# Performance work log

Measured on AMD Instinct MI355X. Metric: run time of the kernel, lower is better.

The kernel has to match this reference:

```python
import jax, jax.numpy as jnp
import numpy as np

B, L, H, NH = 8, 1024, 1024, 16
HD = H // NH  # head_dim = 64
SCALE = HD ** -0.5


def setup_inputs() -> dict:
    key = jax.random.key(0)
    kx, kqkv, kw, kb = jax.random.split(key, 4)
    x = jax.random.normal(kx, (B, L, H), dtype=jnp.float32)
    # nn.Linear(H, 3H, bias=False): weight [3H, H]
    w_qkv = jax.random.normal(kqkv, (3 * H, H), dtype=jnp.float32) * (H ** -0.5)
    # out_proj: nn.Linear(H, H) with bias
    w_out = jax.random.normal(kw, (H, H), dtype=jnp.float32) * (H ** -0.5)
    b_out = jax.random.normal(kb, (H,), dtype=jnp.float32) * 0.01
    return {"x": x, "w_qkv": w_qkv, "w_out": w_out, "b_out": b_out}


def reference(x, w_qkv, w_out, b_out):
    # qkv projection: [B, L, 3H]
    qkv = jnp.einsum('bld,ed->ble', x, w_qkv)
    # rearrange 'b l (qkv h d) -> qkv b h l d'
    qkv = qkv.reshape(B, L, 3, NH, HD)
    q = qkv[:, :, 0].transpose(0, 2, 1, 3)  # [B, NH, L, HD]
    k = qkv[:, :, 1].transpose(0, 2, 1, 3)
    v = qkv[:, :, 2].transpose(0, 2, 1, 3)
    att = jnp.einsum('bhxd,bhyd->bhxy', q, k) * SCALE
    att = jax.nn.softmax(att, axis=-1)
    o = jnp.einsum('bhxy,bhyd->bhxd', att, v)  # [B, NH, L, HD]
    o = o.transpose(0, 2, 1, 3).reshape(B, L, H)
    return jnp.einsum('bld,ed->ble', o, w_out) + b_out
```

## Files before the change

kernel.cpp:

```cpp
#include <hip/hip_runtime.h>


typedef short s16x8 __attribute__((ext_vector_type(8)));
typedef float f32x4 __attribute__((ext_vector_type(4)));
typedef unsigned int u32x2 __attribute__((ext_vector_type(2)));
typedef unsigned int u32x4 __attribute__((ext_vector_type(4)));

__device__ __forceinline__ unsigned short f2bf(float f) {
    union { float f; unsigned u; } c; c.f = f;
    return (unsigned short)((c.u + 0x7FFFu + ((c.u >> 16) & 1u)) >> 16);
}
__device__ __forceinline__ unsigned pack2bf(float a, float b) {
    union { float f; unsigned u; } ca, cb; ca.f = a; cb.f = b;
    return __builtin_amdgcn_perm(cb.u + 0x8000u, ca.u + 0x8000u, 0x07060302u);
}

#define GLOAD_LDS(g, l) __builtin_amdgcn_global_load_lds( \
    (const __attribute__((address_space(1))) void*)(g),   \
    (__attribute__((address_space(3))) void*)(l), 16, 0, 0)

__global__ __launch_bounds__(256) void cvt3(
    const float* __restrict__ s0, unsigned short* __restrict__ d0, int n0,
    const float* __restrict__ s1, unsigned short* __restrict__ d1, int n1,
    const float* __restrict__ s2, unsigned short* __restrict__ d2, int n2)
{
    long i = ((long)blockIdx.x * 256 + threadIdx.x) * 8;
    const float* s; unsigned short* d; long off;
    if (i < n0)                  { s = s0; d = d0; off = i; }
    else if (i < (long)n0 + n1)  { s = s1; d = d1; off = i - n0; }
    else                         { s = s2; d = d2; off = i - n0 - n1; }
    f32x4 a = *(const f32x4*)(s + off);
    f32x4 b = *(const f32x4*)(s + off + 4);
    u32x4 r;
    r[0] = pack2bf(a[0], a[1]); r[1] = pack2bf(a[2], a[3]);
    r[2] = pack2bf(b[0], b[1]); r[3] = pack2bf(b[2], b[3]);
    *(u32x4*)(d + off) = r;
}

template<int EPI>
__global__ __launch_bounds__(256) void gemm16(
    const unsigned short* __restrict__ A, const unsigned short* __restrict__ Bm,
    unsigned short* __restrict__ Cq, unsigned short* __restrict__ Cv,
    float* __restrict__ Cf, const float* __restrict__ bias,
    int N, int K)
{
    __shared__ unsigned short As[128 * 64];
    __shared__ unsigned short Bs[128 * 64];
    const int tid = threadIdx.x, lane = tid & 63, wave = tid >> 6;
    const int quad = lane >> 4, l16 = lane & 15;
    const int wm = (wave >> 1) * 64, wn = (wave & 1) * 64;
    const int m0 = blockIdx.y * 128, n0 = blockIdx.x * 128;

    const int prow = tid >> 3;
    const int qch  = (tid & 7) ^ (prow & 7);
    const unsigned short* gA[4];
    const unsigned short* gB[4];
    #pragma unroll
    for (int c = 0; c < 4; ++c) {
        gA[c] = A + (size_t)(m0 + c * 32 + prow) * K + qch * 8;
        gB[c] = Bm + (size_t)(n0 + c * 32 + prow) * K + qch * 8;
    }
    const int sw = l16 & 7;

    f32x4 acc[4][4] = {};
    for (int k0 = 0; k0 < K; k0 += 64) {
        __syncthreads();
        #pragma unroll
        for (int c = 0; c < 4; ++c) {
            GLOAD_LDS(gA[c], As + (c * 256 + tid) * 8);
            GLOAD_LDS(gB[c], Bs + (c * 256 + tid) * 8);
            gA[c] += 64; gB[c] += 64;
        }
        __syncthreads();
        #pragma unroll
        for (int s = 0; s < 2; ++s) {
            s16x8 af[4], bf[4];
            const int pc = ((s * 4 + quad) ^ sw) * 8;
            #pragma unroll
            for (int i = 0; i < 4; ++i)
                af[i] = *(const s16x8*)(As + (wm + i * 16 + l16) * 64 + pc);
            #pragma unroll
            for (int j = 0; j < 4; ++j)
                bf[j] = *(const s16x8*)(Bs + (wn + j * 16 + l16) * 64 + pc);
            #pragma unroll
            for (int i = 0; i < 4; ++i)
                #pragma unroll
                for (int j = 0; j < 4; ++j)
                    acc[i][j] = __builtin_amdgcn_mfma_f32_16x16x32_bf16(af[i], bf[j], acc[i][j], 0, 0, 0);
        }
    }

    if (EPI == 1) {
        #pragma unroll
        for (int j = 0; j < 4; ++j) {
            int col = n0 + wn + j * 16 + l16;
            float bv = bias[col];
            #pragma unroll
            for (int i = 0; i < 4; ++i)
                #pragma unroll
                for (int r = 0; r < 4; ++r)
                    Cf[(size_t)(m0 + wm + i * 16 + quad * 4 + r) * N + col] = acc[i][j][r] + bv;
        }
    } else if (n0 < 2048) {
        const float qs = (n0 < 1024) ? 0.18033688f : 1.0f;
        #pragma unroll
        for (int j = 0; j < 4; ++j) {
            int col = n0 + wn + j * 16 + l16;
            #pragma unroll
            for (int i = 0; i < 4; ++i)
                #pragma unroll
                for (int r = 0; r < 4; ++r)
                    Cq[(size_t)(m0 + wm + i * 16 + quad * 4 + r) * 2048 + col] = f2bf(acc[i][j][r] * qs);
        }
    } else {
        #pragma unroll
        for (int j = 0; j < 4; ++j) {
            int dcol = n0 + wn + j * 16 + l16 - 2048;
            int hh = dcol >> 6, dd = dcol & 63;
            #pragma unroll
            for (int i = 0; i < 4; ++i) {
                int row = m0 + wm + i * 16 + quad * 4;
                int bb = row >> 10, l = row & 1023;
                u32x2 pw;
                pw[0] = pack2bf(acc[i][j][0], acc[i][j][1]);
                pw[1] = pack2bf(acc[i][j][2], acc[i][j][3]);
                *(u32x2*)(Cv + (size_t)((bb * 16 + hh) * 64 + dd) * 1024 + l) = pw;
            }
        }
    }
}

__global__ __launch_bounds__(256) void attn(
    const unsigned short* __restrict__ qk, const unsigned short* __restrict__ Vt,
    unsigned short* __restrict__ O)
{
    __shared__ unsigned short Ks[64 * 64];
    __shared__ unsigned short Vs[64 * 64];

    const int bh = blockIdx.y, b = bh >> 4, hh = bh & 15;
    const int q0 = blockIdx.x * 64;
    const int tid = threadIdx.x, lane = tid & 63, wave = tid >> 6;
    const int quad = lane >> 4, l16 = lane & 15;

    const unsigned short* qrow =
        qk + (size_t)(b * 1024 + q0 + wave * 16 + l16) * 2048 + hh * 64;
    s16x8 qf[2];
    qf[0] = *(const s16x8*)(qrow + quad * 8);
    qf[1] = *(const s16x8*)(qrow + 32 + quad * 8);

    const int rl = lane >> 3;
    const int qc = (lane & 7) ^ rl;
    const int u0 = rl >> 2, r0 = rl & 3;
    const int kvbase = 32 * (wave >> 1) + 4 * (wave & 1) + r0;
    const int kv0 = kvbase + 8 * u0;
    const int kv1 = kvbase + 8 * (2 + u0);
    const unsigned short* srcK0 = qk + (size_t)(b * 1024 + kv0) * 2048 + 1024 + hh * 64 + qc * 8;
    const unsigned short* srcK1 = qk + (size_t)(b * 1024 + kv1) * 2048 + 1024 + hh * 64 + qc * 8;
    const unsigned short* srcV0 = Vt + (size_t)(bh * 64 + wave * 16 + rl) * 1024 + qc * 8;
    const unsigned short* srcV1 = Vt + (size_t)(bh * 64 + wave * 16 + 8 + rl) * 1024 + qc * 8;
    unsigned short* dK0 = Ks + (wave * 16 + rl) * 64 + (lane & 7) * 8;
    unsigned short* dK1 = Ks + (wave * 16 + 8 + rl) * 64 + (lane & 7) * 8;
    unsigned short* dV0 = Vs + (wave * 16 + rl) * 64 + (lane & 7) * 8;
    unsigned short* dV1 = Vs + (wave * 16 + 8 + rl) * 64 + (lane & 7) * 8;

    const int sw = l16 & 7;

    f32x4 Oacc[4] = {};
    float lsum = 0.0f;

    for (int kv = 0; kv < 1024; kv += 64) {
        __syncthreads();
        GLOAD_LDS(srcK0, dK0);
        GLOAD_LDS(srcK1, dK1);
        GLOAD_LDS(srcV0, dV0);
        GLOAD_LDS(srcV1, dV1);
        srcK0 += (size_t)64 * 2048; srcK1 += (size_t)64 * 2048;
        srcV0 += 64; srcV1 += 64;
        __syncthreads();

        f32x4 Sacc[4] = {};
        #pragma unroll
        for (int t = 0; t < 4; ++t) {
            #pragma unroll
            for (int s = 0; s < 2; ++s) {
                s16x8 kf = *(const s16x8*)(Ks + (t * 16 + l16) * 64 + ((s * 4 + quad) ^ sw) * 8);
                Sacc[t] = __builtin_amdgcn_mfma_f32_16x16x32_bf16(kf, qf[s], Sacc[t], 0, 0, 0);
            }
        }
        unsigned upw[4][2];
        #pragma unroll
        for (int t = 0; t < 4; ++t) {
            float p0 = __builtin_amdgcn_exp2f(Sacc[t][0]);
            float p1 = __builtin_amdgcn_exp2f(Sacc[t][1]);
            float p2 = __builtin_amdgcn_exp2f(Sacc[t][2]);
            float p3 = __builtin_amdgcn_exp2f(Sacc[t][3]);
            lsum += (p0 + p1) + (p2 + p3);
            upw[t][0] = pack2bf(p0, p1);
            upw[t][1] = pack2bf(p2, p3);
        }
        #pragma unroll
        for (int s = 0; s < 2; ++s) {
            u32x4 aw;
            aw[0] = upw[2 * s][0];     aw[1] = upw[2 * s][1];
            aw[2] = upw[2 * s + 1][0]; aw[3] = upw[2 * s + 1][1];
            s16x8 pf;
            __builtin_memcpy(&pf, &aw, 16);
            #pragma unroll
            for (int jd = 0; jd < 4; ++jd) {
                s16x8 vf = *(const s16x8*)(Vs + (jd * 16 + l16) * 64 + ((s * 4 + quad) ^ sw) * 8);
                Oacc[jd] = __builtin_amdgcn_mfma_f32_16x16x32_bf16(pf, vf, Oacc[jd], 0, 0, 0);
            }
        }
    }

    lsum += __shfl_xor(lsum, 16, 64);
    lsum += __shfl_xor(lsum, 32, 64);
    float rinv[4];
    #pragma unroll
    for (int r = 0; r < 4; ++r)
        rinv[r] = 1.0f / __shfl(lsum, quad * 4 + r, 64);
    #pragma unroll
    for (int j = 0; j < 4; ++j)
        #pragma unroll
        for (int r = 0; r < 4; ++r) {
            int row = q0 + wave * 16 + quad * 4 + r;
            int col = hh * 64 + j * 16 + l16;
            O[(size_t)(b * 1024 + row) * 1024 + col] = f2bf(Oacc[j][r] * rinv[r]);
        }
}

extern "C" void kernel_launch(void* const* d_in, const int* in_sizes, int n_in,
                              void* d_out, int out_size, void* d_ws, size_t ws_size,
                              hipStream_t stream) {
    const float* x     = (const float*)d_in[0];
    const float* w_qkv = (const float*)d_in[1];
    const float* w_out = (const float*)d_in[2];
    const float* b_out = (const float*)d_in[3];
    float* out = (float*)d_out;

    const int nx = 8192 * 1024, nwq = 3072 * 1024, nwo = 1024 * 1024;
    unsigned short* xb  = (unsigned short*)d_ws;
    unsigned short* wqb = xb + nx;
    unsigned short* wob = wqb + nwq;
    unsigned short* qkb = wob + nwo;
    unsigned short* Vt  = qkb + (size_t)8192 * 2048;
    unsigned short* Ob  = xb;

    dim3 blk(256);
    cvt3<<<6144, blk, 0, stream>>>(x, xb, nx, w_qkv, wqb, nwq, w_out, wob, nwo);
    gemm16<0><<<dim3(24, 64), blk, 0, stream>>>(xb, wqb, qkb, Vt, nullptr, nullptr, 3072, 1024);
    attn<<<dim3(16, 128), blk, 0, stream>>>(qkb, Vt, Ob);
    gemm16<1><<<dim3(8, 64), blk, 0, stream>>>(Ob, wob, nullptr, nullptr, out, b_out, 1024, 1024);
}
```

Measured before the change: 232.8 us.

## Rewrite GEMMs as 8-wave 256x128 tiles with triple-buffered LDS prefetch pipeline

Replaces the 4-wave 128x128 GEMM with a 512-thread kernel that computes 256x128 tiles and keeps three LDS stages of A and B. Global-to-LDS loads for tile t+2 are issued in two halves interleaved with the MFMA phases, using vmcnt waits and raw barriers instead of full syncthreads. It also remaps workgroup IDs in an XCD-aware way to improve L2 locality, and raises MFMA wave priority with setprio. The intent is to hide memory latency behind the matrix math. In exchange, K is hardcoded to 1024 and LDS use grows to 144 KB per block.

```diff
diff --git a/kernel.cpp b/kernel.cpp
--- a/kernel.cpp
+++ b/kernel.cpp
@@ -38,88 +38,134 @@
 }
 
 template<int EPI>
-__global__ __launch_bounds__(256) void gemm16(
+__global__ __launch_bounds__(512, 2) void gemm8p(
     const unsigned short* __restrict__ A, const unsigned short* __restrict__ Bm,
     unsigned short* __restrict__ Cq, unsigned short* __restrict__ Cv,
-    float* __restrict__ Cf, const float* __restrict__ bias,
-    int N, int K)
+    float* __restrict__ Cf, const float* __restrict__ bias, int N)
 {
-    __shared__ unsigned short As[128 * 64];
-    __shared__ unsigned short Bs[128 * 64];
+    __shared__ unsigned short As[3 * 256 * 64];
+    __shared__ unsigned short Bs[3 * 128 * 64];
     const int tid = threadIdx.x, lane = tid & 63, wave = tid >> 6;
     const int quad = lane >> 4, l16 = lane & 15;
-    const int wm = (wave >> 1) * 64, wn = (wave & 1) * 64;
-    const int m0 = blockIdx.y * 128, n0 = blockIdx.x * 128;
+    const int wr = (wave >> 1) * 64;
+    const int wc = (wave & 1) * 64;
+
+    const int gx = gridDim.x, nwg = gx * gridDim.y;
+    int wg = blockIdx.y * gx + blockIdx.x;
+    wg = (wg & 7) * (nwg >> 3) + (wg >> 3);
+    const int n0 = (wg % gx) * 128, m0 = (wg / gx) * 256;
 
     const int prow = tid >> 3;
     const int qch  = (tid & 7) ^ (prow & 7);
     const unsigned short* gA[4];
-    const unsigned short* gB[4];
-    #pragma unroll
-    for (int c = 0; c < 4; ++c) {
-        gA[c] = A + (size_t)(m0 + c * 32 + prow) * K + qch * 8;
-        gB[c] = Bm + (size_t)(n0 + c * 32 + prow) * K + qch * 8;
-    }
+    const unsigned short* gB[2];
+    #pragma unroll
+    for (int c = 0; c < 4; ++c)
+        gA[c] = A + (size_t)(m0 + c * 64 + prow) * 1024 + qch * 8;
+    #pragma unroll
+    for (int c = 0; c < 2; ++c)
+        gB[c] = Bm + (size_t)(n0 + c * 64 + prow) * 1024 + qch * 8;
+    unsigned short* dA = As + tid * 8;
+    unsigned short* dB = Bs + tid * 8;
+
+    #pragma unroll
+    for (int t = 0; t < 2; ++t) {
+        #pragma unroll
+        for (int c = 0; c < 4; ++c) GLOAD_LDS(gA[c] + t * 64, dA + t * 16384 + c * 4096);
+        #pragma unroll
+        for (int c = 0; c < 2; ++c) GLOAD_LDS(gB[c] + t * 64, dB + t * 8192 + c * 4096);
+    }
+    asm volatile("s_waitcnt vmcnt(6)" ::: "memory");
+    __builtin_amdgcn_s_barrier();
+
+    f32x4 acc[4][4] = {};
     const int sw = l16 & 7;
-
-    f32x4 acc[4][4] = {};
-    for (int k0 = 0; k0 < K; k0 += 64) {
-        __syncthreads();
-        #pragma unroll
-        for (int c = 0; c < 4; ++c) {
-            GLOAD_LDS(gA[c], As + (c * 256 + tid) * 8);
-            GLOAD_LDS(gB[c], Bs + (c * 256 + tid) * 8);
-            gA[c] += 64; gB[c] += 64;
-        }
-        __syncthreads();
-        #pragma unroll
-        for (int s = 0; s < 2; ++s) {
-            s16x8 af[4], bf[4];
-            const int pc = ((s * 4 + quad) ^ sw) * 8;
-            #pragma unroll
-            for (int i = 0; i < 4; ++i)
-                af[i] = *(const s16x8*)(As + (wm + i * 16 + l16) * 64 + pc);
+    int rA = 0, rB = 0;
+    int r2A = 2 * 16384, r2B = 2 * 8192;
+    for (int t = 0; t < 16; ++t) {
+        const unsigned short* pa = As + rA + (wr + l16) * 64;
+        const unsigned short* pb = Bs + rB + (wc + l16) * 64;
+        s16x8 af[4], bf[4];
+        {
+            const int pc = (quad ^ sw) * 8;
+            #pragma unroll
+            for (int i = 0; i < 4; ++i) af[i] = *(const s16x8*)(pa + i * 1024 + pc);
+            #pragma unroll
+            for (int j = 0; j < 4; ++j) bf[j] = *(const s16x8*)(pb + j * 1024 + pc);
+        }
+        if (t < 14) {
+            GLOAD_LDS(gA[0] + (t + 2) * 64, dA + r2A);
+            GLOAD_LDS(gA[1] + (t + 2) * 64, dA + r2A + 4096);
+            GLOAD_LDS(gA[2] + (t + 2) * 64, dA + r2A + 8192);
+        }
+        __builtin_amdgcn_s_barrier();
+        __builtin_amdgcn_s_setprio(1);
+        #pragma unroll
+        for (int i = 0; i < 4; ++i)
             #pragma unroll
             for (int j = 0; j < 4; ++j)
-                bf[j] = *(const s16x8*)(Bs + (wn + j * 16 + l16) * 64 + pc);
-            #pragma unroll
-            for (int i = 0; i < 4; ++i)
-                #pragma unroll
-                for (int j = 0; j < 4; ++j)
-                    acc[i][j] = __builtin_amdgcn_mfma_f32_16x16x32_bf16(af[i], bf[j], acc[i][j], 0, 0, 0);
-        }
+                acc[i][j] = __builtin_amdgcn_mfma_f32_16x16x32_bf16(af[i], bf[j], acc[i][j], 0, 0, 0);
+        __builtin_amdgcn_s_setprio(0);
+        __builtin_amdgcn_s_barrier();
+        {
+            const int pc = ((4 + quad) ^ sw) * 8;
+            #pragma unroll
+            for (int i = 0; i < 4; ++i) af[i] = *(const s16x8*)(pa + i * 1024 + pc);
+            #pragma unroll
+            for (int j = 0; j < 4; ++j) bf[j] = *(const s16x8*)(pb + j * 1024 + pc);
+        }
+        if (t < 14) {
+            GLOAD_LDS(gA[3] + (t + 2) * 64, dA + r2A + 12288);
+            GLOAD_LDS(gB[0] + (t + 2) * 64, dB + r2B);
+            GLOAD_LDS(gB[1] + (t + 2) * 64, dB + r2B + 4096);
+        }
+        __builtin_amdgcn_s_barrier();
+        __builtin_amdgcn_s_setprio(1);
+        #pragma unroll
+        for (int i = 0; i < 4; ++i)
+            #pragma unroll
+            for (int j = 0; j < 4; ++j)
+                acc[i][j] = __builtin_amdgcn_mfma_f32_16x16x32_bf16(af[i], bf[j], acc[i][j], 0, 0, 0);
+        __builtin_amdgcn_s_setprio(0);
+        if (t < 14)       asm volatile("s_waitcnt vmcnt(6)" ::: "memory");
+        else if (t == 14) asm volatile("s_waitcnt vmcnt(0)" ::: "memory");
+        __builtin_amdgcn_s_barrier();
+        rA  = (rA  == 2 * 16384) ? 0 : rA  + 16384;
+        rB  = (rB  == 2 * 8192)  ? 0 : rB  + 8192;
+        r2A = (r2A == 2 * 16384) ? 0 : r2A + 16384;
+        r2B = (r2B == 2 * 8192)  ? 0 : r2B + 8192;
     }
 
     if (EPI == 1) {
         #pragma unroll
         for (int j = 0; j < 4; ++j) {
-            int col = n0 + wn + j * 16 + l16;
+            int col = n0 + wc + j * 16 + l16;
             float bv = bias[col];
             #pragma unroll
             for (int i = 0; i < 4; ++i)
                 #pragma unroll
                 for (int r = 0; r < 4; ++r)
-                    Cf[(size_t)(m0 + wm + i * 16 + quad * 4 + r) * N + col] = acc[i][j][r] + bv;
+                    Cf[(size_t)(m0 + wr + i * 16 + quad * 4 + r) * N + col] = acc[i][j][r] + bv;
         }
     } else if (n0 < 2048) {
         const float qs = (n0 < 1024) ? 0.18033688f : 1.0f;
         #pragma unroll
         for (int j = 0; j < 4; ++j) {
-            int col = n0 + wn + j * 16 + l16;
+            int col = n0 + wc + j * 16 + l16;
             #pragma unroll
             for (int i = 0; i < 4; ++i)
                 #pragma unroll
                 for (int r = 0; r < 4; ++r)
-                    Cq[(size_t)(m0 + wm + i * 16 + quad * 4 + r) * 2048 + col] = f2bf(acc[i][j][r] * qs);
+                    Cq[(size_t)(m0 + wr + i * 16 + quad * 4 + r) * 2048 + col] = f2bf(acc[i][j][r] * qs);
         }
     } else {
         #pragma unroll
         for (int j = 0; j < 4; ++j) {
-            int dcol = n0 + wn + j * 16 + l16 - 2048;
+            int dcol = n0 + wc + j * 16 + l16 - 2048;
             int hh = dcol >> 6, dd = dcol & 63;
             #pragma unroll
             for (int i = 0; i < 4; ++i) {
-                int row = m0 + wm + i * 16 + quad * 4;
+                int row = m0 + wr + i * 16 + quad * 4;
                 int bb = row >> 10, l = row & 1023;
                 u32x2 pw;
                 pw[0] = pack2bf(acc[i][j][0], acc[i][j][1]);
@@ -246,9 +292,8 @@
     unsigned short* Vt  = qkb + (size_t)8192 * 2048;
     unsigned short* Ob  = xb;
 
-    dim3 blk(256);
-    cvt3<<<6144, blk, 0, stream>>>(x, xb, nx, w_qkv, wqb, nwq, w_out, wob, nwo);
-    gemm16<0><<<dim3(24, 64), blk, 0, stream>>>(xb, wqb, qkb, Vt, nullptr, nullptr, 3072, 1024);
-    attn<<<dim3(16, 128), blk, 0, stream>>>(qkb, Vt, Ob);
-    gemm16<1><<<dim3(8, 64), blk, 0, stream>>>(Ob, wob, nullptr, nullptr, out, b_out, 1024, 1024);
-}
+    cvt3<<<6144, dim3(256), 0, stream>>>(x, xb, nx, w_qkv, wqb, nwq, w_out, wob, nwo);
+    gemm8p<0><<<dim3(24, 32), dim3(512), 0, stream>>>(xb, wqb, qkb, Vt, nullptr, nullptr, 3072);
+    attn<<<dim3(16, 128), dim3(256), 0, stream>>>(qkb, Vt, Ob);
+    gemm8p<1><<<dim3(8, 32), dim3(512), 0, stream>>>(Ob, wob, nullptr, nullptr, out, b_out, 1024);
+}
```

After: 234.7 us. No clear change (+0.8%).

## Replace GEMMs with 256x256 double-buffered 8-wave pipelined MFMA kernel

Applied to the files above, without the earlier changes.

Both projection GEMMs move from 128x128 tiles with 4 waves and a single LDS buffer to 256x256 tiles with 8 waves, double-buffered LDS, and global-to-LDS loads for the next tiles interleaved between MFMA quarter-steps. The quarter-steps are separated by barriers and run with raised wave priority during MFMA. Workgroup IDs are remapped so consecutive IDs are spread across eight groups, which is meant to improve cache locality. The goal is to hide load latency and raise operand reuse per load. The cost is 128KB of LDS per block, fewer blocks (128 for the out projection, below the CU count), and K hardcoded to 1024.

```diff
diff --git a/kernel.cpp b/kernel.cpp
--- a/kernel.cpp
+++ b/kernel.cpp
@@ -38,92 +38,157 @@
 }
 
 template<int EPI>
-__global__ __launch_bounds__(256) void gemm16(
+__global__ __launch_bounds__(512, 2) void gemm8p(
     const unsigned short* __restrict__ A, const unsigned short* __restrict__ Bm,
     unsigned short* __restrict__ Cq, unsigned short* __restrict__ Cv,
-    float* __restrict__ Cf, const float* __restrict__ bias,
-    int N, int K)
+    float* __restrict__ Cf, const float* __restrict__ bias, int Nout)
 {
-    __shared__ unsigned short As[128 * 64];
-    __shared__ unsigned short Bs[128 * 64];
+    __shared__ unsigned short As[2 * 256 * 64];
+    __shared__ unsigned short Bs[2 * 256 * 64];
     const int tid = threadIdx.x, lane = tid & 63, wave = tid >> 6;
     const int quad = lane >> 4, l16 = lane & 15;
-    const int wm = (wave >> 1) * 64, wn = (wave & 1) * 64;
-    const int m0 = blockIdx.y * 128, n0 = blockIdx.x * 128;
+    const int wm = wave >> 2;
+    const int wn = wave & 3;
+
+    const int gx = gridDim.x, nwg = gx * gridDim.y;
+    int wg = blockIdx.y * gx + blockIdx.x;
+    wg = (wg & 7) * (nwg >> 3) + (wg >> 3);
+    const int n0 = (wg % gx) * 256, m0 = (wg / gx) * 256;
 
     const int prow = tid >> 3;
     const int qch  = (tid & 7) ^ (prow & 7);
-    const unsigned short* gA[4];
-    const unsigned short* gB[4];
-    #pragma unroll
-    for (int c = 0; c < 4; ++c) {
-        gA[c] = A + (size_t)(m0 + c * 32 + prow) * K + qch * 8;
-        gB[c] = Bm + (size_t)(n0 + c * 32 + prow) * K + qch * 8;
+    const unsigned short* baseA = A  + (size_t)(m0 + prow) * 1024 + qch * 8;
+    const unsigned short* baseB = Bm + (size_t)(n0 + prow) * 1024 + qch * 8;
+    unsigned short* dA = As + tid * 8;
+    unsigned short* dB = Bs + tid * 8;
+
+    auto STGA = [&](int t, int h, int c) {
+        GLOAD_LDS(baseA + (h * 128 + c * 64) * 1024 + t * 64,
+                  dA + (t & 1) * 16384 + h * 8192 + c * 4096);
+    };
+    auto STGB = [&](int t, int h, int c) {
+        GLOAD_LDS(baseB + (h * 128 + c * 64) * 1024 + t * 64,
+                  dB + (t & 1) * 16384 + h * 8192 + c * 4096);
+    };
+
+    STGA(0, 0, 0); STGA(0, 0, 1);
+    STGB(0, 0, 0); STGB(0, 0, 1);
+    STGB(0, 1, 0); STGB(0, 1, 1);
+    STGA(0, 1, 0); STGA(0, 1, 1);
+    STGA(1, 0, 0); STGA(1, 0, 1);
+    STGB(1, 0, 0); STGB(1, 0, 1);
+    STGB(1, 1, 0); STGB(1, 1, 1);
+    asm volatile("s_waitcnt vmcnt(6)" ::: "memory");
+    __builtin_amdgcn_s_barrier();
+
+    f32x4 acc[8][4] = {};
+    s16x8 af[4][2];
+    s16x8 bf[2][2][2];
+    const int sw = l16 & 7;
+
+    auto LDA = [&](int P, int mh) {
+        #pragma unroll
+        for (int mf = 0; mf < 4; ++mf)
+            #pragma unroll
+            for (int kk = 0; kk < 2; ++kk)
+                af[mf][kk] = *(const s16x8*)(As + P * 16384 +
+                    (mh * 128 + wm * 64 + mf * 16 + l16) * 64 +
+                    ((kk * 4 + quad) ^ sw) * 8);
+    };
+    auto LDB = [&](int P, int nh) {
+        #pragma unroll
+        for (int nf = 0; nf < 2; ++nf)
+            #pragma unroll
+            for (int kk = 0; kk < 2; ++kk)
+                bf[nh][nf][kk] = *(const s16x8*)(Bs + P * 16384 +
+                    (wn * 64 + (nh * 2 + nf) * 16 + l16) * 64 +
+                    ((kk * 4 + quad) ^ sw) * 8);
+    };
+    auto MM = [&](int mh, int nh) {
+        __builtin_amdgcn_s_setprio(1);
+        #pragma unroll
+        for (int mf = 0; mf < 4; ++mf)
+            #pragma unroll
+            for (int nf = 0; nf < 2; ++nf)
+                #pragma unroll
+                for (int kk = 0; kk < 2; ++kk)
+                    acc[mh * 4 + mf][nh * 2 + nf] =
+                        __builtin_amdgcn_mfma_f32_16x16x32_bf16(
+                            af[mf][kk], bf[nh][nf][kk],
+                            acc[mh * 4 + mf][nh * 2 + nf], 0, 0, 0);
+        __builtin_amdgcn_s_setprio(0);
+    };
+
+    auto TILE = [&](int t, int smode) {
+        const int P = t & 1;
+        LDA(P, 0); LDB(P, 0);
+        if (smode >= 1) { STGA(t + 1, 1, 0); STGA(t + 1, 1, 1); }
+        __builtin_amdgcn_s_barrier();
+        MM(0, 0);
+        __builtin_amdgcn_s_barrier();
+        LDB(P, 1);
+        if (smode == 2) { STGA(t + 2, 0, 0); STGA(t + 2, 0, 1); }
+        __builtin_amdgcn_s_barrier();
+        MM(0, 1);
+        __builtin_amdgcn_s_barrier();
+        LDA(P, 1);
+        if (smode == 2) { STGB(t + 2, 0, 0); STGB(t + 2, 0, 1); }
+        __builtin_amdgcn_s_barrier();
+        MM(1, 1);
+        __builtin_amdgcn_s_barrier();
+        if (smode == 2) { STGB(t + 2, 1, 0); STGB(t + 2, 1, 1); }
+        __builtin_amdgcn_s_barrier();
+        MM(1, 0);
+        if (smode == 2)      asm volatile("s_waitcnt vmcnt(6)" ::: "memory");
+        else if (smode == 1) asm volatile("s_waitcnt vmcnt(0)" ::: "memory");
+        __builtin_amdgcn_s_barrier();
+    };
+
+    for (int t2 = 0; t2 < 7; ++t2) {
+        TILE(2 * t2,     2);
+        TILE(2 * t2 + 1, 2);
     }
-    const int sw = l16 & 7;
-
-    f32x4 acc[4][4] = {};
-    for (int k0 = 0; k0 < K; k0 += 64) {
-        __syncthreads();
-        #pragma unroll
-        for (int c = 0; c < 4; ++c) {
-            GLOAD_LDS(gA[c], As + (c * 256 + tid) * 8);
-            GLOAD_LDS(gB[c], Bs + (c * 256 + tid) * 8);
-            gA[c] += 64; gB[c] += 64;
-        }
-        __syncthreads();
-        #pragma unroll
-        for (int s = 0; s < 2; ++s) {
-            s16x8 af[4], bf[4];
-            const int pc = ((s * 4 + quad) ^ sw) * 8;
-            #pragma unroll
-            for (int i = 0; i < 4; ++i)
-                af[i] = *(const s16x8*)(As + (wm + i * 16 + l16) * 64 + pc);
-            #pragma unroll
-            for (int j = 0; j < 4; ++j)
-                bf[j] = *(const s16x8*)(Bs + (wn + j * 16 + l16) * 64 + pc);
-            #pragma unroll
-            for (int i = 0; i < 4; ++i)
-                #pragma unroll
-                for (int j = 0; j < 4; ++j)
-                    acc[i][j] = __builtin_amdgcn_mfma_f32_16x16x32_bf16(af[i], bf[j], acc[i][j], 0, 0, 0);
-        }
-    }
+    TILE(14, 1);
+    TILE(15, 0);
 
     if (EPI == 1) {
         #pragma unroll
-        for (int j = 0; j < 4; ++j) {
-            int col = n0 + wn + j * 16 + l16;
+        for (int nj = 0; nj < 4; ++nj) {
+            int col = n0 + wn * 64 + nj * 16 + l16;
             float bv = bias[col];
             #pragma unroll
-            for (int i = 0; i < 4; ++i)
+            for (int mi = 0; mi < 8; ++mi) {
+                int row = m0 + (mi >> 2) * 128 + wm * 64 + (mi & 3) * 16 + quad * 4;
                 #pragma unroll
                 for (int r = 0; r < 4; ++r)
-                    Cf[(size_t)(m0 + wm + i * 16 + quad * 4 + r) * N + col] = acc[i][j][r] + bv;
+                    Cf[(size_t)(row + r) * Nout + col] = acc[mi][nj][r] + bv;
+            }
         }
     } else if (n0 < 2048) {
         const float qs = (n0 < 1024) ? 0.18033688f : 1.0f;
         #pragma unroll
-        for (int j = 0; j < 4; ++j) {
-            int col = n0 + wn + j * 16 + l16;
-            #pragma unroll
-            for (int i = 0; i < 4; ++i)
+        for (int nj = 0; nj < 4; ++nj) {
+            int col = n0 + wn * 64 + nj * 16 + l16;
+            #pragma unroll
+            for (int mi = 0; mi < 8; ++mi) {
+                int row = m0 + (mi >> 2) * 128 + wm * 64 + (mi & 3) * 16 + quad * 4;
                 #pragma unroll
                 for (int r = 0; r < 4; ++r)
-                    Cq[(size_t)(m0 + wm + i * 16 + quad * 4 + r) * 2048 + col] = f2bf(acc[i][j][r] * qs);
+                    Cq[(size_t)(row + r) * 2048 + col] = f2bf(acc[mi][nj][r] * qs);
+            }
         }
     } else {
         #pragma unroll
-        for (int j = 0; j < 4; ++j) {
-            int dcol = n0 + wn + j * 16 + l16 - 2048;
+        for (int nj = 0; nj < 4; ++nj) {
+            int dcol = n0 + wn * 64 + nj * 16 + l16 - 2048;
             int hh = dcol >> 6, dd = dcol & 63;
             #pragma unroll
-            for (int i = 0; i < 4; ++i) {
-                int row = m0 + wm + i * 16 + quad * 4;
+            for (int mi = 0; mi < 8; ++mi) {
+                int row = m0 + (mi >> 2) * 128 + wm * 64 + (mi & 3) * 16 + quad * 4;
                 int bb = row >> 10, l = row & 1023;
                 u32x2 pw;
-                pw[0] = pack2bf(acc[i][j][0], acc[i][j][1]);
-                pw[1] = pack2bf(acc[i][j][2], acc[i][j][3]);
+                pw[0] = pack2bf(acc[mi][nj][0], acc[mi][nj][1]);
+                pw[1] = pack2bf(acc[mi][nj][2], acc[mi][nj][3]);
                 *(u32x2*)(Cv + (size_t)((bb * 16 + hh) * 64 + dd) * 1024 + l) = pw;
             }
         }
@@ -246,9 +311,8 @@
     unsigned short* Vt  = qkb + (size_t)8192 * 2048;
     unsigned short* Ob  = xb;
 
-    dim3 blk(256);
-    cvt3<<<6144, blk, 0, stream>>>(x, xb, nx, w_qkv, wqb, nwq, w_out, wob, nwo);
-    gemm16<0><<<dim3(24, 64), blk, 0, stream>>>(xb, wqb, qkb, Vt, nullptr, nullptr, 3072, 1024);
-    attn<<<dim3(16, 128), blk, 0, stream>>>(qkb, Vt, Ob);
-    gemm16<1><<<dim3(8, 64), blk, 0, stream>>>(Ob, wob, nullptr, nullptr, out, b_out, 1024, 1024);
-}
+    cvt3<<<6144, dim3(256), 0, stream>>>(x, xb, nx, w_qkv, wqb, nwq, w_out, wob, nwo);
+    gemm8p<0><<<dim3(12, 32), dim3(512), 0, stream>>>(xb, wqb, qkb, Vt, nullptr, nullptr, 3072);
+    attn<<<dim3(16, 128), dim3(256), 0, stream>>>(qkb, Vt, Ob);
+    gemm8p<1><<<dim3(4, 32), dim3(512), 0, stream>>>(Ob, wob, nullptr, nullptr, out, b_out, 1024);
+}
```

Result: slower. 256.3 us (+10.1%).

## Process two query blocks per wave in attention to reuse K/V tiles

Applied to the files above, without the earlier changes.

Each attention workgroup now handles 128 query rows instead of 64, with every wave holding two 16-row query fragments. Each K and V fragment read from LDS feeds two MFMAs, halving K/V global loads and LDS reads per query row and halving the grid. s_setprio hints are also added around the MFMA sections. The cost is higher register use, a possible drop in occupancy, and half as many workgroups (1024) to fill the CUs.

```diff
diff --git a/kernel.cpp b/kernel.cpp
--- a/kernel.cpp
+++ b/kernel.cpp
@@ -138,15 +138,18 @@
     __shared__ unsigned short Vs[64 * 64];
 
     const int bh = blockIdx.y, b = bh >> 4, hh = bh & 15;
-    const int q0 = blockIdx.x * 64;
+    const int q0 = blockIdx.x * 128;
     const int tid = threadIdx.x, lane = tid & 63, wave = tid >> 6;
     const int quad = lane >> 4, l16 = lane & 15;
 
-    const unsigned short* qrow =
-        qk + (size_t)(b * 1024 + q0 + wave * 16 + l16) * 2048 + hh * 64;
-    s16x8 qf[2];
-    qf[0] = *(const s16x8*)(qrow + quad * 8);
-    qf[1] = *(const s16x8*)(qrow + 32 + quad * 8);
+    s16x8 qf[2][2];
+    #pragma unroll
+    for (int qb = 0; qb < 2; ++qb) {
+        const unsigned short* qrow =
+            qk + (size_t)(b * 1024 + q0 + wave * 32 + qb * 16 + l16) * 2048 + hh * 64;
+        qf[qb][0] = *(const s16x8*)(qrow + quad * 8);
+        qf[qb][1] = *(const s16x8*)(qrow + 32 + quad * 8);
+    }
 
     const int rl = lane >> 3;
     const int qc = (lane & 7) ^ rl;
@@ -165,8 +168,8 @@
 
     const int sw = l16 & 7;
 
-    f32x4 Oacc[4] = {};
-    float lsum = 0.0f;
+    f32x4 Oacc[4][2] = {};
+    float lsum[2] = {0.0f, 0.0f};
 
     for (int kv = 0; kv < 1024; kv += 64) {
         __syncthreads();
@@ -178,55 +181,73 @@
         srcV0 += 64; srcV1 += 64;
         __syncthreads();
 
-        f32x4 Sacc[4] = {};
+        f32x4 Sacc[4][2] = {};
+        __builtin_amdgcn_s_setprio(1);
         #pragma unroll
         for (int t = 0; t < 4; ++t) {
             #pragma unroll
             for (int s = 0; s < 2; ++s) {
                 s16x8 kf = *(const s16x8*)(Ks + (t * 16 + l16) * 64 + ((s * 4 + quad) ^ sw) * 8);
-                Sacc[t] = __builtin_amdgcn_mfma_f32_16x16x32_bf16(kf, qf[s], Sacc[t], 0, 0, 0);
-            }
-        }
-        unsigned upw[4][2];
+                #pragma unroll
+                for (int qb = 0; qb < 2; ++qb)
+                    Sacc[t][qb] = __builtin_amdgcn_mfma_f32_16x16x32_bf16(kf, qf[qb][s], Sacc[t][qb], 0, 0, 0);
+            }
+        }
+        __builtin_amdgcn_s_setprio(0);
+        unsigned upw[4][2][2];
         #pragma unroll
         for (int t = 0; t < 4; ++t) {
-            float p0 = __builtin_amdgcn_exp2f(Sacc[t][0]);
-            float p1 = __builtin_amdgcn_exp2f(Sacc[t][1]);
-            float p2 = __builtin_amdgcn_exp2f(Sacc[t][2]);
-            float p3 = __builtin_amdgcn_exp2f(Sacc[t][3]);
-            lsum += (p0 + p1) + (p2 + p3);
-            upw[t][0] = pack2bf(p0, p1);
-            upw[t][1] = pack2bf(p2, p3);
-        }
+            #pragma unroll
+            for (int qb = 0; qb < 2; ++qb) {
+                float p0 = __builtin_amdgcn_exp2f(Sacc[t][qb][0]);
+                float p1 = __builtin_amdgcn_exp2f(Sacc[t][qb][1]);
+                float p2 = __builtin_amdgcn_exp2f(Sacc[t][qb][2]);
+                float p3 = __builtin_amdgcn_exp2f(Sacc[t][qb][3]);
+                lsum[qb] += (p0 + p1) + (p2 + p3);
+                upw[t][qb][0] = pack2bf(p0, p1);
+                upw[t][qb][1] = pack2bf(p2, p3);
+            }
+        }
+        __builtin_amdgcn_s_setprio(1);
         #pragma unroll
         for (int s = 0; s < 2; ++s) {
-            u32x4 aw;
-            aw[0] = upw[2 * s][0];     aw[1] = upw[2 * s][1];
-            aw[2] = upw[2 * s + 1][0]; aw[3] = upw[2 * s + 1][1];
-            s16x8 pf;
-            __builtin_memcpy(&pf, &aw, 16);
+            s16x8 pf[2];
+            #pragma unroll
+            for (int qb = 0; qb < 2; ++qb) {
+                u32x4 aw;
+                aw[0] = upw[2 * s][qb][0];     aw[1] = upw[2 * s][qb][1];
+                aw[2] = upw[2 * s + 1][qb][0]; aw[3] = upw[2 * s + 1][qb][1];
+                __builtin_memcpy(&pf[qb], &aw, 16);
+            }
             #pragma unroll
             for (int jd = 0; jd < 4; ++jd) {
                 s16x8 vf = *(const s16x8*)(Vs + (jd * 16 + l16) * 64 + ((s * 4 + quad) ^ sw) * 8);
-                Oacc[jd] = __builtin_amdgcn_mfma_f32_16x16x32_bf16(pf, vf, Oacc[jd], 0, 0, 0);
-            }
-        }
-    }
-
-    lsum += __shfl_xor(lsum, 16, 64);
-    lsum += __shfl_xor(lsum, 32, 64);
-    float rinv[4];
+                #pragma unroll
+                for (int qb = 0; qb < 2; ++qb)
+                    Oacc[jd][qb] = __builtin_amdgcn_mfma_f32_16x16x32_bf16(pf[qb], vf, Oacc[jd][qb], 0, 0, 0);
+            }
+        }
+        __builtin_amdgcn_s_setprio(0);
+    }
+
     #pragma unroll
-    for (int r = 0; r < 4; ++r)
-        rinv[r] = 1.0f / __shfl(lsum, quad * 4 + r, 64);
-    #pragma unroll
-    for (int j = 0; j < 4; ++j)
-        #pragma unroll
-        for (int r = 0; r < 4; ++r) {
-            int row = q0 + wave * 16 + quad * 4 + r;
-            int col = hh * 64 + j * 16 + l16;
-            O[(size_t)(b * 1024 + row) * 1024 + col] = f2bf(Oacc[j][r] * rinv[r]);
-        }
+    for (int qb = 0; qb < 2; ++qb) {
+        float ls = lsum[qb];
+        ls += __shfl_xor(ls, 16, 64);
+        ls += __shfl_xor(ls, 32, 64);
+        float rinv[4];
+        #pragma unroll
+        for (int r = 0; r < 4; ++r)
+            rinv[r] = 1.0f / __shfl(ls, quad * 4 + r, 64);
+        #pragma unroll
+        for (int j = 0; j < 4; ++j)
+            #pragma unroll
+            for (int r = 0; r < 4; ++r) {
+                int row = q0 + wave * 32 + qb * 16 + quad * 4 + r;
+                int col = hh * 64 + j * 16 + l16;
+                O[(size_t)(b * 1024 + row) * 1024 + col] = f2bf(Oacc[j][qb][r] * rinv[r]);
+            }
+    }
 }
 
 extern "C" void kernel_launch(void* const* d_in, const int* in_sizes, int n_in,
@@ -249,6 +270,6 @@
     dim3 blk(256);
     cvt3<<<6144, blk, 0, stream>>>(x, xb, nx, w_qkv, wqb, nwq, w_out, wob, nwo);
     gemm16<0><<<dim3(24, 64), blk, 0, stream>>>(xb, wqb, qkb, Vt, nullptr, nullptr, 3072, 1024);
-    attn<<<dim3(16, 128), blk, 0, stream>>>(qkb, Vt, Ob);
+    attn<<<dim3(8, 128), blk, 0, stream>>>(qkb, Vt, Ob);
     gemm16<1><<<dim3(8, 64), blk, 0, stream>>>(Ob, wob, nullptr, nullptr, out, b_out, 1024, 1024);
 }
```

Measured after the change: 244.2 us. 1.05x slower.
